# Optimization experiments

Measured on AMD Instinct MI355X. Metric: run time of the kernel, lower is better.

Reference implementation:

```python
import jax, jax.numpy as jnp
import numpy as np

BN_EPS = 1e-5


def setup_inputs() -> dict:
    key = jax.random.key(0)
    ks = jax.random.split(key, 11)
    B, C, Ci, D, H, W = 2, 256, 128, 8, 32, 32
    s = 0.02  # weight init scale
    return {
        "x": jax.random.normal(ks[0], (B, C, D, H, W), dtype=jnp.float32),
        "Wt": jax.random.normal(ks[1], (Ci, C), dtype=jnp.float32) * s,
        "bt": jax.random.normal(ks[2], (Ci,), dtype=jnp.float32) * s,
        "Wp": jax.random.normal(ks[3], (Ci, C), dtype=jnp.float32) * s,
        "bp": jax.random.normal(ks[4], (Ci,), dtype=jnp.float32) * s,
        "Wg": jax.random.normal(ks[5], (Ci, C), dtype=jnp.float32) * s,
        "bg": jax.random.normal(ks[6], (Ci,), dtype=jnp.float32) * s,
        "Ww": jax.random.normal(ks[7], (C, Ci), dtype=jnp.float32) * s,
        "bw": jax.random.normal(ks[8], (C,), dtype=jnp.float32) * s,
        "gamma": jax.random.normal(ks[9], (C,), dtype=jnp.float32),
        "beta": jax.random.normal(ks[10], (C,), dtype=jnp.float32),
    }


def reference(x, Wt, bt, Wp, bp, Wg, bg, Ww, bw, gamma, beta):
    # x: [B, C, D, H, W]; 1x1x1 Conv3d == per-position channel GEMM.
    B, C, D, H, W = x.shape
    xf = x.reshape(B, C, -1)  # [B, C, N], N = D*H*W

    theta = jnp.einsum('oc,bcn->bno', Wt, xf) + bt          # [B, N, Ci]
    phi = jnp.einsum('oc,bcn->bon', Wp, xf) + bp[None, :, None]  # [B, Ci, N]
    g = jnp.einsum('oc,bcn->bno', Wg, xf) + bg              # [B, N, Ci]

    # Unscaled, unmasked full self-attention over all N spatial positions.
    f = jnp.einsum('bnc,bcm->bnm', theta, phi)              # [B, N, N]
    a = jax.nn.softmax(f, axis=-1)
    y = jnp.einsum('bnm,bmc->bcn', a, g)                    # [B, Ci, N]

    # Output projection W: conv1x1 then BatchNorm3d (training-mode batch stats).
    wy = jnp.einsum('oc,bcn->bon', Ww, y) + bw[None, :, None]  # [B, C, N]
    mean = jnp.mean(wy, axis=(0, 2), keepdims=True)
    var = jnp.var(wy, axis=(0, 2), keepdims=True)
    wy_bn = (wy - mean) * jax.lax.rsqrt(var + BN_EPS)
    wy_bn = wy_bn * gamma[None, :, None] + beta[None, :, None]

    return wy_bn.reshape(B, C, D, H, W) + x
```

## Files before the change

kernel.cpp:

```cpp
#include <hip/hip_runtime.h>
#include <cstdint>
#include <cstddef>


typedef unsigned short u16;
typedef __bf16 bf16x8 __attribute__((ext_vector_type(8)));
typedef float f32x4 __attribute__((ext_vector_type(4)));
typedef float f32x16 __attribute__((ext_vector_type(16)));
typedef unsigned short u16x8 __attribute__((ext_vector_type(8)));

#define B_ 2
#define C_ 256
#define CI_ 128
#define N_ 8192
#define KVB 64

static __device__ __forceinline__ u16 f2bf(float f){
  unsigned u = __builtin_bit_cast(unsigned, f);
  unsigned r = (u + 0x7FFFu + ((u>>16)&1u)) >> 16;
  return (u16)r;
}
static __device__ __forceinline__ float bf2f(u16 v){
  unsigned u = ((unsigned)v) << 16;
  return __builtin_bit_cast(float, u);
}
static __device__ __forceinline__ float fexp2(float x){
  return __builtin_amdgcn_exp2f(x);
}
static __device__ __forceinline__ f32x4 f4zero(){
  f32x4 v; v[0]=0.f; v[1]=0.f; v[2]=0.f; v[3]=0.f; return v;
}
static __device__ __forceinline__ f32x16 f16zero(){
  f32x16 v;
#pragma unroll
  for (int i=0;i<16;i++) v[i]=0.f;
  return v;
}
static __device__ __forceinline__ f32x4 mfma16(bf16x8 a, bf16x8 b, f32x4 c){
  return __builtin_amdgcn_mfma_f32_16x16x32_bf16(a, b, c, 0, 0, 0);
}
static __device__ __forceinline__ f32x16 mfma32(bf16x8 a, bf16x8 b, f32x16 c){
  return __builtin_amdgcn_mfma_f32_32x32x16_bf16(a, b, c, 0, 0, 0);
}
static __device__ __forceinline__ unsigned cvtpk(float lo, float hi){
  unsigned r;
  asm("v_cvt_pk_bf16_f32 %0, %1, %2" : "=v"(r) : "v"(lo), "v"(hi));
  return r;
}
static __device__ __forceinline__ void plswap(unsigned &a, unsigned &b){
  asm volatile("v_permlane32_swap_b32 %0, %1" : "+v"(a), "+v"(b));
}

#define LOG2E 1.4426950408889634f

__global__ void k0_prep(const float* __restrict__ Wt, const float* __restrict__ Wp,
                        const float* __restrict__ Wg, const float* __restrict__ Ww,
                        const float* __restrict__ bt, const float* __restrict__ bp,
                        const float* __restrict__ bg,
                        u16* __restrict__ Wcat, u16* __restrict__ Wwb,
                        float* __restrict__ biasc, float* __restrict__ stats){
  int t = blockIdx.x*blockDim.x + threadIdx.x;
  int nthr = gridDim.x*blockDim.x;
  for (int i = t; i < 32768; i += nthr){
    Wcat[i]        = f2bf(Wt[i] * LOG2E);
    Wcat[32768+i]  = f2bf(Wp[i]);
    Wcat[65536+i]  = f2bf(Wg[i]);
    Wwb[i]         = f2bf(Ww[i]);
  }
  for (int i = t; i < 128; i += nthr){
    biasc[i] = bt[i] * LOG2E; biasc[128+i] = bp[i]; biasc[256+i] = bg[i];
  }
  for (int i = t; i < 512; i += nthr) stats[i] = 0.f;
}

__global__ __launch_bounds__(256) void k1_proj(const float* __restrict__ x,
     const u16* __restrict__ Wcat, const float* __restrict__ biasc,
     u16* __restrict__ theta, u16* __restrict__ kproj, u16* __restrict__ gT){
  __shared__ u16 At[64*264];
  __shared__ u16 Wt_[32*264];
  __shared__ u16 gbuf[32*72];
  int tid = threadIdx.x;
  int b  = blockIdx.x >> 7;
  int nb = (blockIdx.x & 127) * 64;
  int w = tid >> 6, lane = tid & 63;
  int l15 = lane & 15, kg = lane >> 4;

  {
    int cp = tid & 127, nh = tid >> 7;
    int c0 = cp*2;
    const float* src0 = x + ((size_t)(b*C_ + c0))*N_ + nb + nh*32;
    const float* src1 = src0 + N_;
#pragma unroll
    for (int j=0;j<8;j++){
      f32x4 a = *(const f32x4*)(src0 + j*4);
      f32x4 c = *(const f32x4*)(src1 + j*4);
#pragma unroll
      for (int q=0;q<4;q++){
        unsigned pk = (unsigned)f2bf(a[q]) | ((unsigned)f2bf(c[q])<<16);
        *(unsigned*)&At[(nh*32 + j*4 + q)*264 + c0] = pk;
      }
    }
  }
  __syncthreads();

  bf16x8 afr[8];
#pragma unroll
  for (int kc=0;kc<8;kc++)
    afr[kc] = *(const bf16x8*)&At[(w*16+l15)*264 + kc*32 + kg*8];

  for (int och = 0; och < 12; och++){
    {
      int o8 = tid>>3, cp8 = tid&7;
      const u16* wsrc = Wcat + ((size_t)(och*32 + o8))*256 + cp8*8;
#pragma unroll
      for (int j=0;j<4;j++)
        *(u16x8*)&Wt_[o8*264 + cp8*8 + j*64] = *(const u16x8*)(wsrc + j*64);
    }
    __syncthreads();

    f32x4 acc0 = f4zero(), acc1 = f4zero();
#pragma unroll
    for (int kc=0;kc<8;kc++){
      bf16x8 b0 = *(const bf16x8*)&Wt_[(l15)*264 + kc*32 + kg*8];
      bf16x8 b1 = *(const bf16x8*)&Wt_[(16+l15)*264 + kc*32 + kg*8];
      acc0 = mfma16(afr[kc], b0, acc0);
      acc1 = mfma16(afr[kc], b1, acc1);
    }

    if (och < 8){
      u16* dst = (och < 4) ? theta : kproj;
      int oo = (och & 3) * 32;
#pragma unroll
      for (int of=0;of<2;of++){
        int o = oo + of*16 + l15;
        float bias = biasc[och*32 + of*16 + l15];
        f32x4 acc = of ? acc1 : acc0;
#pragma unroll
        for (int i=0;i<4;i++){
          int n = nb + w*16 + kg*4 + i;
          dst[((size_t)b*N_ + n)*CI_ + o] = f2bf(acc[i] + bias);
        }
      }
      __syncthreads();
    } else {
#pragma unroll
      for (int of=0;of<2;of++){
        int o = of*16 + l15;
        float bias = biasc[och*32 + of*16 + l15];
        f32x4 acc = of ? acc1 : acc0;
#pragma unroll
        for (int i=0;i<4;i++){
          int r = w*16 + kg*4 + i;
          gbuf[o*72 + r] = f2bf(acc[i] + bias);
        }
      }
      __syncthreads();
      {
        int o = tid>>3, np = tid&7;
        int og = (och-8)*32 + o;
        u16x8 v = *(const u16x8*)&gbuf[o*72 + np*8];
        *(u16x8*)(gT + ((size_t)b*CI_ + og)*N_ + nb + np*8) = v;
      }
      __syncthreads();
    }
  }
}

__global__ __launch_bounds__(512, 2) void k2_attn(const u16* __restrict__ theta,
      const u16* __restrict__ kproj, const u16* __restrict__ gT,
      u16* __restrict__ pO, float* __restrict__ pM, float* __restrict__ pL){
  constexpr int CHUNK_N = 2048;
  constexpr int NTI = CHUNK_N / KVB;
  __shared__ char smem[65536];
  char* kbase = smem;
  char* vbase = smem + 32768;
  int tid = threadIdx.x;
  int bid = blockIdx.x;
  int combo = bid & 7;
  int b = combo & 1;
  int chunk = combo >> 1;
  int qblk = bid >> 3;
  int n0 = chunk * CHUNK_N;
  int w = tid >> 6, lane = tid & 63;
  int l31 = lane & 31, hi = lane >> 5;
  int qg = qblk*256 + w*32 + l31;

  bf16x8 qf[8];
  {
    const u16* qsrc = theta + ((size_t)b*N_ + qg)*CI_ + hi*8;
#pragma unroll
    for (int cc=0; cc<8; cc++) qf[cc] = *(const bf16x8*)(qsrc + cc*16);
  }

  int krow_s = tid >> 3, kpart = tid & 7;
  int vrow_s = tid >> 2, vpart = tid & 3;
  const u16* ksrc = kproj + ((size_t)b*N_ + n0 + krow_s)*CI_ + kpart*16;
  const u16* vsrc = gT + ((size_t)b*CI_ + vrow_s)*N_ + n0 + vpart*16;
  int kw_off[2], vw_off[2];
#pragma unroll
  for (int j=0;j<2;j++){
    int cb = kpart*32 + j*16;
    kw_off[j] = krow_s*256 + (cb ^ ((krow_s&15)<<4));
    int kb = vpart*32 + j*16;
    vw_off[j] = vrow_s*128 + (kb ^ ((vrow_s&7)<<4));
  }
  int kswz = (l31&15)<<4;
  int vswz = (l31&7)<<4;
  int kro[8], vro[4];
#pragma unroll
  for (int cc=0;cc<8;cc++) kro[cc] = l31*256 + ((cc*32 + hi*16) ^ kswz);
#pragma unroll
  for (int ks=0;ks<4;ks++) vro[ks] = l31*128 + ((ks*32 + hi*16) ^ vswz);

#pragma unroll
  for (int j=0;j<2;j++){
    *(u16x8*)(kbase + kw_off[j]) = *(const u16x8*)(ksrc + j*8);
    *(u16x8*)(vbase + vw_off[j]) = *(const u16x8*)(vsrc + j*8);
  }
  __syncthreads();

  f32x16 oacc[4];
#pragma unroll
  for (int i=0;i<4;i++) oacc[i] = f16zero();
  float mrun = -1e30f, lrun = 0.f;

  for (int t=0; t<NTI; t++){
    int cur = t & 1;
    char* kb_c = kbase + cur*16384;
    char* vb_c = vbase + cur*16384;
    u16x8 kst[2], vst[2];
    bool pf = (t+1 < NTI);
    if (pf){
      const u16* ks = ksrc + (size_t)(t+1)*KVB*CI_;
      const u16* vs = vsrc + (t+1)*KVB;
#pragma unroll
      for (int j=0;j<2;j++) kst[j] = *(const u16x8*)(ks + j*8);
#pragma unroll
      for (int j=0;j<2;j++) vst[j] = *(const u16x8*)(vs + j*8);
    }

    f32x16 sA = f16zero(), sB = f16zero();
    __builtin_amdgcn_s_setprio(1);
#pragma unroll
    for (int cc=0; cc<8; cc++){
      bf16x8 kf0 = *(const bf16x8*)(kb_c + kro[cc]);
      bf16x8 kf1 = *(const bf16x8*)(kb_c + 8192 + kro[cc]);
      sA = mfma32(kf0, qf[cc], sA);
      sB = mfma32(kf1, qf[cc], sB);
    }
    __builtin_amdgcn_s_setprio(0);

    float t8[8];
#pragma unroll
    for (int i=0;i<8;i++) t8[i] = fmaxf(fmaxf(sA[i], sA[i+8]), fmaxf(sB[i], sB[i+8]));
    float m4a = fmaxf(t8[0], t8[4]), m4b = fmaxf(t8[1], t8[5]);
    float m4c = fmaxf(t8[2], t8[6]), m4d = fmaxf(t8[3], t8[7]);
    float mx = fmaxf(fmaxf(m4a, m4b), fmaxf(m4c, m4d));
    mx = fmaxf(mx, __shfl_xor(mx, 32));
    if (__any(mx > mrun + 12.f)){
      float mnew = fmaxf(mrun, mx);
      float sc = fexp2(mrun - mnew);
      lrun *= sc;
#pragma unroll
      for (int i=0;i<4;i++)
#pragma unroll
        for (int r=0;r<16;r++) oacc[i][r] *= sc;
      mrun = mnew;
    }
    float pA[16], pB[16];
#pragma unroll
    for (int r=0;r<16;r++){ pA[r] = fexp2(sA[r]-mrun); pB[r] = fexp2(sB[r]-mrun); }
    float s8[8];
#pragma unroll
    for (int i=0;i<8;i++) s8[i] = (pA[i]+pA[i+8]) + (pB[i]+pB[i+8]);
    float s4a = s8[0]+s8[4], s4b = s8[1]+s8[5], s4c = s8[2]+s8[6], s4d = s8[3]+s8[7];
    float ps = (s4a+s4b) + (s4c+s4d);
    ps += __shfl_xor(ps, 32);
    lrun += ps;

    if (pf){
      char* kd = kbase + (cur^1)*16384;
      char* vd = vbase + (cur^1)*16384;
#pragma unroll
      for (int j=0;j<2;j++) *(u16x8*)(kd + kw_off[j]) = kst[j];
#pragma unroll
      for (int j=0;j<2;j++) *(u16x8*)(vd + vw_off[j]) = vst[j];
    }

    __builtin_amdgcn_s_setprio(1);
#pragma unroll
    for (int ks=0; ks<4; ks++){
      const float* P = (ks<2) ? pA : pB;
      int r0 = (ks&1)*8;
      unsigned a0 = cvtpk(P[r0+0], P[r0+1]);
      unsigned b0 = cvtpk(P[r0+4], P[r0+5]);
      unsigned a1 = cvtpk(P[r0+2], P[r0+3]);
      unsigned b1 = cvtpk(P[r0+6], P[r0+7]);
      plswap(a0, b0); plswap(a1, b1);
      union { unsigned u[4]; bf16x8 v; } pb;
      pb.u[0]=a0; pb.u[1]=a1; pb.u[2]=b0; pb.u[3]=b1;
#pragma unroll
      for (int c2=0; c2<4; c2++){
        bf16x8 vf = *(const bf16x8*)(vb_c + c2*4096 + vro[ks]);
        oacc[c2] = mfma32(vf, pb.v, oacc[c2]);
      }
    }
    __builtin_amdgcn_s_setprio(0);
    __syncthreads();
  }

  char* region = smem + w*8192;
#pragma unroll
  for (int c2=0;c2<4;c2++)
#pragma unroll
    for (int r=0;r<16;r++){
      int c = c2*32 + (r&3) + 8*(r>>2) + 4*hi;
      *(u16*)(region + l31*256 + ((c*2) ^ vswz)) = f2bf(oacc[c2][r]);
    }
  __syncthreads();
  {
    int ql = lane >> 1, half = lane & 1;
    int qg2 = qblk*256 + w*32 + ql;
    u16* dst = pO + ((size_t)(chunk*2 + b)*N_ + qg2)*CI_ + half*64;
    int rswz = (ql&7)<<4;
#pragma unroll
    for (int j=0;j<8;j++){
      u16x8 v2 = *(const u16x8*)(region + ql*256 + ((half*128 + j*16) ^ rswz));
      *(u16x8*)(dst + j*8) = v2;
    }
  }
  if (hi == 0){
    pM[(size_t)(chunk*2 + b)*N_ + qg] = mrun;
    pL[(size_t)(chunk*2 + b)*N_ + qg] = lrun;
  }
}

__global__ __launch_bounds__(256) void k3_wy(const u16* __restrict__ pO,
    const float* __restrict__ pM, const float* __restrict__ pL,
    const u16* __restrict__ Wwb, const float* __restrict__ bw,
    u16* __restrict__ wy, float* __restrict__ stats){
  __shared__ u16 Yt[64*136];
  __shared__ u16 Wt_[64*136];
  __shared__ float wyb[64*72];
  int tid = threadIdx.x;
  int b  = blockIdx.x >> 7;
  int nb = (blockIdx.x & 127) * 64;
  int w = tid>>6, lane = tid&63;
  int l15 = lane&15, kg = lane>>4;

  {
    int n = tid>>2, cp = tid&3;
    size_t q = (size_t)nb + n;
    float m[4], l[4];
#pragma unroll
    for (int ch=0; ch<4; ch++){
      m[ch] = pM[(size_t)(ch*2+b)*N_ + q];
      l[ch] = pL[(size_t)(ch*2+b)*N_ + q];
    }
    float M = fmaxf(fmaxf(m[0],m[1]), fmaxf(m[2],m[3]));
    float wts[4]; float L = 0.f;
#pragma unroll
    for (int ch=0; ch<4; ch++){ wts[ch] = exp2f(m[ch]-M); L += wts[ch]*l[ch]; }
    float inv = 1.f/L;
#pragma unroll
    for (int j=0;j<4;j++){
      int c0 = cp*32 + j*8;
      float acc[8];
#pragma unroll
      for (int i=0;i<8;i++) acc[i]=0.f;
#pragma unroll
      for (int ch=0; ch<4; ch++){
        u16x8 v = *(const u16x8*)(pO + ((size_t)(ch*2+b)*N_ + q)*CI_ + c0);
#pragma unroll
        for (int i=0;i<8;i++) acc[i] += wts[ch]*bf2f(v[i]);
      }
#pragma unroll
      for (int i=0;i<4;i++){
        unsigned pk = (unsigned)f2bf(acc[2*i]*inv) | ((unsigned)f2bf(acc[2*i+1]*inv)<<16);
        *(unsigned*)&Yt[n*136 + c0 + 2*i] = pk;
      }
    }
  }
  __syncthreads();

  bf16x8 afr[4];
#pragma unroll
  for (int kc=0;kc<4;kc++)
    afr[kc] = *(const bf16x8*)&Yt[(w*16+l15)*136 + kc*32 + kg*8];

  for (int oc=0; oc<4; oc++){
    {
      int o = tid>>2, cp = tid&3;
      const u16* src = Wwb + ((size_t)(oc*64 + o))*CI_ + cp*32;
#pragma unroll
      for (int j=0;j<4;j++)
        *(u16x8*)&Wt_[o*136 + cp*32 + j*8] = *(const u16x8*)(src + j*8);
    }
    __syncthreads();

    f32x4 acc[4];
#pragma unroll
    for (int of=0;of<4;of++) acc[of] = f4zero();
#pragma unroll
    for (int kc=0;kc<4;kc++){
#pragma unroll
      for (int of=0;of<4;of++){
        bf16x8 bfr = *(const bf16x8*)&Wt_[(of*16+l15)*136 + kc*32 + kg*8];
        acc[of] = mfma16(afr[kc], bfr, acc[of]);
      }
    }
#pragma unroll
    for (int of=0;of<4;of++){
#pragma unroll
      for (int i=0;i<4;i++)
        wyb[(of*16+l15)*72 + w*16 + kg*4 + i] = acc[of][i];
    }
    __syncthreads();
    {
      int o = tid>>2, np = tid&3;
      int og = oc*64 + o;
      float bias = bw[og];
      float sm = 0.f, sq = 0.f;
      u16* dst = wy + ((size_t)b*C_ + og)*N_ + nb + np*16;
      u16 buf[16];
#pragma unroll
      for (int j=0;j<4;j++){
#pragma unroll
        for (int q2=0;q2<4;q2++){
          float t2 = wyb[o*72 + np*16 + j*4 + q2] + bias;
          buf[j*4+q2] = f2bf(t2); sm += t2; sq += t2*t2;
        }
      }
      *(u16x8*)dst = *(const u16x8*)&buf[0];
      *(u16x8*)(dst+8) = *(const u16x8*)&buf[8];
      sm += __shfl_xor(sm, 1); sm += __shfl_xor(sm, 2);
      sq += __shfl_xor(sq, 1); sq += __shfl_xor(sq, 2);
      if ((tid&3)==0){
        atomicAdd(&stats[og], sm);
        atomicAdd(&stats[256+og], sq);
      }
    }
    __syncthreads();
  }
}

__global__ __launch_bounds__(256) void k4_bn(const u16* __restrict__ wy,
    const float* __restrict__ x, const float* __restrict__ stats,
    const float* __restrict__ gamma, const float* __restrict__ beta,
    float* __restrict__ out){
  size_t base = ((size_t)blockIdx.x)*2048 + (size_t)threadIdx.x*8;
  int o = (int)((base >> 13) & 255);
  const float invn = 1.f/16384.f;
  float mean = stats[o]*invn;
  float var  = stats[256+o]*invn - mean*mean;
  float rs = rsqrtf(var + 1e-5f);
  float g = gamma[o]*rs;
  float bb = beta[o];
  u16x8 a = *(const u16x8*)(wy + base);
  f32x4 x0 = *(const f32x4*)(x + base);
  f32x4 x1 = *(const f32x4*)(x + base + 4);
  f32x4 r0, r1;
#pragma unroll
  for (int q=0;q<4;q++){
    r0[q] = (bf2f(a[q])-mean)*g + bb + x0[q];
    r1[q] = (bf2f(a[4+q])-mean)*g + bb + x1[q];
  }
  *(f32x4*)(out + base)     = r0;
  *(f32x4*)(out + base + 4) = r1;
}

extern "C" void kernel_launch(void* const* d_in, const int* in_sizes, int n_in,
                              void* d_out, int out_size, void* d_ws, size_t ws_size,
                              hipStream_t stream){
  const float* x     = (const float*)d_in[0];
  const float* Wt    = (const float*)d_in[1];
  const float* bt    = (const float*)d_in[2];
  const float* Wp    = (const float*)d_in[3];
  const float* bp    = (const float*)d_in[4];
  const float* Wg    = (const float*)d_in[5];
  const float* bg    = (const float*)d_in[6];
  const float* Ww    = (const float*)d_in[7];
  const float* bw    = (const float*)d_in[8];
  const float* gamma = (const float*)d_in[9];
  const float* beta  = (const float*)d_in[10];

  char* ws = (char*)d_ws;
  u16*   theta = (u16*)(ws + 0);
  u16*   kproj = (u16*)(ws + 4194304);
  u16*   gT    = (u16*)(ws + 8388608);
  u16*   pO    = (u16*)(ws + 12582912);
  float* pM    = (float*)(ws + 29360128);
  float* pL    = (float*)(ws + 29622272);
  u16*   wy    = (u16*)(ws + 29884416);
  u16*   Wcat  = (u16*)(ws + 38273024);
  u16*   Wwb   = (u16*)(ws + 38469632);
  float* biasc = (float*)(ws + 38535168);
  float* stats = (float*)(ws + 38536704);
  float* out   = (float*)d_out;

  k0_prep<<<64, 256, 0, stream>>>(Wt, Wp, Wg, Ww, bt, bp, bg, Wcat, Wwb, biasc, stats);
  k1_proj<<<256, 256, 0, stream>>>(x, Wcat, biasc, theta, kproj, gT);
  k2_attn<<<256, 512, 0, stream>>>(theta, kproj, gT, pO, pM, pL);
  k3_wy<<<256, 256, 0, stream>>>(pO, pM, pL, Wwb, bw, wy, stats);
  k4_bn<<<2048, 256, 0, stream>>>(wy, x, stats, gamma, beta, out);
}
```

Baseline: 131.9 us.

## Software-pipeline attention loop across tiles and fold weight prep into consumers

```diff
diff --git a/kernel.cpp b/kernel.cpp
--- a/kernel.cpp
+++ b/kernel.cpp
@@ -53,29 +53,12 @@
 
 #define LOG2E 1.4426950408889634f
 
-__global__ void k0_prep(const float* __restrict__ Wt, const float* __restrict__ Wp,
-                        const float* __restrict__ Wg, const float* __restrict__ Ww,
-                        const float* __restrict__ bt, const float* __restrict__ bp,
-                        const float* __restrict__ bg,
-                        u16* __restrict__ Wcat, u16* __restrict__ Wwb,
-                        float* __restrict__ biasc, float* __restrict__ stats){
-  int t = blockIdx.x*blockDim.x + threadIdx.x;
-  int nthr = gridDim.x*blockDim.x;
-  for (int i = t; i < 32768; i += nthr){
-    Wcat[i]        = f2bf(Wt[i] * LOG2E);
-    Wcat[32768+i]  = f2bf(Wp[i]);
-    Wcat[65536+i]  = f2bf(Wg[i]);
-    Wwb[i]         = f2bf(Ww[i]);
-  }
-  for (int i = t; i < 128; i += nthr){
-    biasc[i] = bt[i] * LOG2E; biasc[128+i] = bp[i]; biasc[256+i] = bg[i];
-  }
-  for (int i = t; i < 512; i += nthr) stats[i] = 0.f;
-}
-
 __global__ __launch_bounds__(256) void k1_proj(const float* __restrict__ x,
-     const u16* __restrict__ Wcat, const float* __restrict__ biasc,
-     u16* __restrict__ theta, u16* __restrict__ kproj, u16* __restrict__ gT){
+     const float* __restrict__ Wt, const float* __restrict__ Wp,
+     const float* __restrict__ Wg, const float* __restrict__ bt,
+     const float* __restrict__ bp, const float* __restrict__ bg,
+     u16* __restrict__ theta, u16* __restrict__ kproj, u16* __restrict__ gT,
+     float* __restrict__ stats){
   __shared__ u16 At[64*264];
   __shared__ u16 Wt_[32*264];
   __shared__ u16 gbuf[32*72];
@@ -85,6 +68,10 @@
   int w = tid >> 6, lane = tid & 63;
   int l15 = lane & 15, kg = lane >> 4;
 
+  if (blockIdx.x == 0){
+    stats[tid] = 0.f; stats[256 + tid] = 0.f;
+  }
+
   {
     int cp = tid & 127, nh = tid >> 7;
     int c0 = cp*2;
@@ -111,10 +98,19 @@
   for (int och = 0; och < 12; och++){
     {
       int o8 = tid>>3, cp8 = tid&7;
-      const u16* wsrc = Wcat + ((size_t)(och*32 + o8))*256 + cp8*8;
-#pragma unroll
-      for (int j=0;j<4;j++)
-        *(u16x8*)&Wt_[o8*264 + cp8*8 + j*64] = *(const u16x8*)(wsrc + j*64);
+      const float* wsel = (och<4) ? (Wt + ((size_t)(och*32 + o8))*256)
+                        : (och<8) ? (Wp + ((size_t)((och-4)*32 + o8))*256)
+                                  : (Wg + ((size_t)((och-8)*32 + o8))*256);
+      float scl = (och<4) ? LOG2E : 1.f;
+#pragma unroll
+      for (int j=0;j<4;j++){
+        f32x4 w0 = *(const f32x4*)(wsel + cp8*8 + j*64);
+        f32x4 w1 = *(const f32x4*)(wsel + cp8*8 + j*64 + 4);
+        u16 tmp[8];
+#pragma unroll
+        for (int q=0;q<4;q++){ tmp[q] = f2bf(w0[q]*scl); tmp[4+q] = f2bf(w1[q]*scl); }
+        *(u16x8*)&Wt_[o8*264 + cp8*8 + j*64] = *(const u16x8*)tmp;
+      }
     }
     __syncthreads();
 
@@ -133,7 +129,8 @@
 #pragma unroll
       for (int of=0;of<2;of++){
         int o = oo + of*16 + l15;
-        float bias = biasc[och*32 + of*16 + l15];
+        float bias = (och<4) ? bt[och*32 + of*16 + l15] * LOG2E
+                             : bp[(och-4)*32 + of*16 + l15];
         f32x4 acc = of ? acc1 : acc0;
 #pragma unroll
         for (int i=0;i<4;i++){
@@ -146,7 +143,7 @@
 #pragma unroll
       for (int of=0;of<2;of++){
         int o = of*16 + l15;
-        float bias = biasc[och*32 + of*16 + l15];
+        float bias = bg[(och-8)*32 + of*16 + l15];
         f32x4 acc = of ? acc1 : acc0;
 #pragma unroll
         for (int i=0;i<4;i++){
@@ -171,9 +168,7 @@
       u16* __restrict__ pO, float* __restrict__ pM, float* __restrict__ pL){
   constexpr int CHUNK_N = 2048;
   constexpr int NTI = CHUNK_N / KVB;
-  __shared__ char smem[65536];
-  char* kbase = smem;
-  char* vbase = smem + 32768;
+  __shared__ char smem[81920];
   int tid = threadIdx.x;
   int bid = blockIdx.x;
   int combo = bid & 7;
@@ -185,6 +180,12 @@
   int l31 = lane & 31, hi = lane >> 5;
   int qg = qblk*256 + w*32 + l31;
 
+  char* kb_cur = smem;
+  char* kb_nxt = smem + 16384;
+  char* vb_cur = smem + 32768;
+  char* vb_nxt = smem + 49152;
+  char* vb_prev = smem + 65536;
+
   bf16x8 qf[8];
   {
     const u16* qsrc = theta + ((size_t)b*N_ + qg)*CI_ + hi*8;
@@ -214,8 +215,8 @@
 
 #pragma unroll
   for (int j=0;j<2;j++){
-    *(u16x8*)(kbase + kw_off[j]) = *(const u16x8*)(ksrc + j*8);
-    *(u16x8*)(vbase + vw_off[j]) = *(const u16x8*)(vsrc + j*8);
+    *(u16x8*)(kb_cur + kw_off[j]) = *(const u16x8*)(ksrc + j*8);
+    *(u16x8*)(vb_cur + vw_off[j]) = *(const u16x8*)(vsrc + j*8);
   }
   __syncthreads();
 
@@ -223,91 +224,108 @@
 #pragma unroll
   for (int i=0;i<4;i++) oacc[i] = f16zero();
   float mrun = -1e30f, lrun = 0.f;
-
-  for (int t=0; t<NTI; t++){
-    int cur = t & 1;
-    char* kb_c = kbase + cur*16384;
-    char* vb_c = vbase + cur*16384;
-    u16x8 kst[2], vst[2];
-    bool pf = (t+1 < NTI);
-    if (pf){
-      const u16* ks = ksrc + (size_t)(t+1)*KVB*CI_;
-      const u16* vs = vsrc + (t+1)*KVB;
-#pragma unroll
-      for (int j=0;j<2;j++) kst[j] = *(const u16x8*)(ks + j*8);
-#pragma unroll
-      for (int j=0;j<2;j++) vst[j] = *(const u16x8*)(vs + j*8);
-    }
-
-    f32x16 sA = f16zero(), sB = f16zero();
-    __builtin_amdgcn_s_setprio(1);
-#pragma unroll
-    for (int cc=0; cc<8; cc++){
-      bf16x8 kf0 = *(const bf16x8*)(kb_c + kro[cc]);
-      bf16x8 kf1 = *(const bf16x8*)(kb_c + 8192 + kro[cc]);
-      sA = mfma32(kf0, qf[cc], sA);
-      sB = mfma32(kf1, qf[cc], sB);
-    }
+  f32x16 sA0, sB0, sA1, sB1;
+
+#define K2_ROT() { char* _t = vb_prev; vb_prev = vb_cur; vb_cur = vb_nxt; vb_nxt = _t; \
+                   char* _k = kb_cur; kb_cur = kb_nxt; kb_nxt = _k; }
+
+#define K2_MAX(CA, CB) { float t8[8]; \
+    _Pragma("unroll") \
+    for (int i=0;i<8;i++) t8[i] = fmaxf(fmaxf(CA[i], CA[i+8]), fmaxf(CB[i], CB[i+8])); \
+    float mx = fmaxf(fmaxf(fmaxf(t8[0],t8[4]),fmaxf(t8[1],t8[5])), \
+                     fmaxf(fmaxf(t8[2],t8[6]),fmaxf(t8[3],t8[7]))); \
+    mx = fmaxf(mx, __shfl_xor(mx, 32)); \
+    if (__any(mx > mrun + 12.f)){ \
+      float mnew = fmaxf(mrun, mx); \
+      float sc = fexp2(mrun - mnew); \
+      lrun *= sc; \
+      _Pragma("unroll") \
+      for (int i=0;i<4;i++){ _Pragma("unroll") for (int r=0;r<16;r++) oacc[i][r] *= sc; } \
+      mrun = mnew; } }
+
+#define K2_EXP(PA, PB, pA, pB) \
+    float pA[16], pB[16]; \
+    _Pragma("unroll") \
+    for (int r=0;r<16;r++){ pA[r] = fexp2(PA[r]-mrun); pB[r] = fexp2(PB[r]-mrun); } \
+    { float s8[8]; \
+      _Pragma("unroll") \
+      for (int i=0;i<8;i++) s8[i] = (pA[i]+pA[i+8]) + (pB[i]+pB[i+8]); \
+      float ps = ((s8[0]+s8[4])+(s8[1]+s8[5])) + ((s8[2]+s8[6])+(s8[3]+s8[7])); \
+      ps += __shfl_xor(ps, 32); lrun += ps; }
+
+#define K2_PV(pA, pB) \
+    __builtin_amdgcn_s_setprio(1); \
+    _Pragma("unroll") \
+    for (int ks=0; ks<4; ks++){ \
+      const float* P = (ks<2) ? pA : pB; \
+      int r0 = (ks&1)*8; \
+      unsigned a0 = cvtpk(P[r0+0], P[r0+1]); \
+      unsigned b0 = cvtpk(P[r0+4], P[r0+5]); \
+      unsigned a1 = cvtpk(P[r0+2], P[r0+3]); \
+      unsigned b1 = cvtpk(P[r0+6], P[r0+7]); \
+      plswap(a0, b0); plswap(a1, b1); \
+      union { unsigned u[4]; bf16x8 v; } pb; \
+      pb.u[0]=a0; pb.u[1]=a1; pb.u[2]=b0; pb.u[3]=b1; \
+      _Pragma("unroll") \
+      for (int c2=0; c2<4; c2++){ \
+        bf16x8 vf = *(const bf16x8*)(vb_prev + c2*4096 + vro[ks]); \
+        oacc[c2] = mfma32(vf, pb.v, oacc[c2]); \
+      } \
+    } \
     __builtin_amdgcn_s_setprio(0);
 
-    float t8[8];
-#pragma unroll
-    for (int i=0;i<8;i++) t8[i] = fmaxf(fmaxf(sA[i], sA[i+8]), fmaxf(sB[i], sB[i+8]));
-    float m4a = fmaxf(t8[0], t8[4]), m4b = fmaxf(t8[1], t8[5]);
-    float m4c = fmaxf(t8[2], t8[6]), m4d = fmaxf(t8[3], t8[7]);
-    float mx = fmaxf(fmaxf(m4a, m4b), fmaxf(m4c, m4d));
-    mx = fmaxf(mx, __shfl_xor(mx, 32));
-    if (__any(mx > mrun + 12.f)){
-      float mnew = fmaxf(mrun, mx);
-      float sc = fexp2(mrun - mnew);
-      lrun *= sc;
-#pragma unroll
-      for (int i=0;i<4;i++)
-#pragma unroll
-        for (int r=0;r<16;r++) oacc[i][r] *= sc;
-      mrun = mnew;
-    }
-    float pA[16], pB[16];
-#pragma unroll
-    for (int r=0;r<16;r++){ pA[r] = fexp2(sA[r]-mrun); pB[r] = fexp2(sB[r]-mrun); }
-    float s8[8];
-#pragma unroll
-    for (int i=0;i<8;i++) s8[i] = (pA[i]+pA[i+8]) + (pB[i]+pB[i+8]);
-    float s4a = s8[0]+s8[4], s4b = s8[1]+s8[5], s4c = s8[2]+s8[6], s4d = s8[3]+s8[7];
-    float ps = (s4a+s4b) + (s4c+s4d);
-    ps += __shfl_xor(ps, 32);
-    lrun += ps;
-
-    if (pf){
-      char* kd = kbase + (cur^1)*16384;
-      char* vd = vbase + (cur^1)*16384;
-#pragma unroll
-      for (int j=0;j<2;j++) *(u16x8*)(kd + kw_off[j]) = kst[j];
-#pragma unroll
-      for (int j=0;j<2;j++) *(u16x8*)(vd + vw_off[j]) = vst[j];
-    }
-
-    __builtin_amdgcn_s_setprio(1);
-#pragma unroll
-    for (int ks=0; ks<4; ks++){
-      const float* P = (ks<2) ? pA : pB;
-      int r0 = (ks&1)*8;
-      unsigned a0 = cvtpk(P[r0+0], P[r0+1]);
-      unsigned b0 = cvtpk(P[r0+4], P[r0+5]);
-      unsigned a1 = cvtpk(P[r0+2], P[r0+3]);
-      unsigned b1 = cvtpk(P[r0+6], P[r0+7]);
-      plswap(a0, b0); plswap(a1, b1);
-      union { unsigned u[4]; bf16x8 v; } pb;
-      pb.u[0]=a0; pb.u[1]=a1; pb.u[2]=b0; pb.u[3]=b1;
-#pragma unroll
-      for (int c2=0; c2<4; c2++){
-        bf16x8 vf = *(const bf16x8*)(vb_c + c2*4096 + vro[ks]);
-        oacc[c2] = mfma32(vf, pb.v, oacc[c2]);
-      }
-    }
+#define K2_QKT(CA, CB) \
+    CA = f16zero(); CB = f16zero(); \
+    __builtin_amdgcn_s_setprio(1); \
+    _Pragma("unroll") \
+    for (int cc=0; cc<8; cc++){ \
+      bf16x8 kf0 = *(const bf16x8*)(kb_cur + kro[cc]); \
+      bf16x8 kf1 = *(const bf16x8*)(kb_cur + 8192 + kro[cc]); \
+      CA = mfma32(kf0, qf[cc], CA); \
+      CB = mfma32(kf1, qf[cc], CB); \
+    } \
     __builtin_amdgcn_s_setprio(0);
+
+#define K2_LOADS(T) \
+    int tn = ((T)+1 < NTI) ? ((T)+1) : (NTI-1); \
+    u16x8 kst0 = *(const u16x8*)(ksrc + (size_t)tn*KVB*CI_); \
+    u16x8 kst1 = *(const u16x8*)(ksrc + (size_t)tn*KVB*CI_ + 8); \
+    u16x8 vst0 = *(const u16x8*)(vsrc + tn*KVB); \
+    u16x8 vst1 = *(const u16x8*)(vsrc + tn*KVB + 8);
+
+#define K2_WRITES() \
+    *(u16x8*)(kb_nxt + kw_off[0]) = kst0; *(u16x8*)(kb_nxt + kw_off[1]) = kst1; \
+    *(u16x8*)(vb_nxt + vw_off[0]) = vst0; *(u16x8*)(vb_nxt + vw_off[1]) = vst1;
+
+#define K2_ITER(T, CA, CB, PA, PB) { \
+    K2_LOADS(T) \
+    K2_QKT(CA, CB) \
+    K2_EXP(PA, PB, pA_, pB_) \
+    K2_WRITES() \
+    K2_PV(pA_, pB_) \
+    K2_MAX(CA, CB) \
+    __syncthreads(); \
+    K2_ROT() }
+
+  {
+    K2_LOADS(0)
+    K2_QKT(sA0, sB0)
+    K2_WRITES()
+    K2_MAX(sA0, sB0)
     __syncthreads();
-  }
+    K2_ROT()
+  }
+  for (int t = 1; t < NTI-1; t += 2){
+    K2_ITER(t,   sA1, sB1, sA0, sB0)
+    K2_ITER(t+1, sA0, sB0, sA1, sB1)
+  }
+  K2_ITER(NTI-1, sA1, sB1, sA0, sB0)
+
+  {
+    K2_EXP(sA1, sB1, pA_, pB_)
+    K2_PV(pA_, pB_)
+  }
+  __syncthreads();
 
   char* region = smem + w*8192;
 #pragma unroll
@@ -337,7 +355,7 @@
 
 __global__ __launch_bounds__(256) void k3_wy(const u16* __restrict__ pO,
     const float* __restrict__ pM, const float* __restrict__ pL,
-    const u16* __restrict__ Wwb, const float* __restrict__ bw,
+    const float* __restrict__ Ww, const float* __restrict__ bw,
     u16* __restrict__ wy, float* __restrict__ stats){
   __shared__ u16 Yt[64*136];
   __shared__ u16 Wt_[64*136];
@@ -391,10 +409,16 @@
   for (int oc=0; oc<4; oc++){
     {
       int o = tid>>2, cp = tid&3;
-      const u16* src = Wwb + ((size_t)(oc*64 + o))*CI_ + cp*32;
-#pragma unroll
-      for (int j=0;j<4;j++)
-        *(u16x8*)&Wt_[o*136 + cp*32 + j*8] = *(const u16x8*)(src + j*8);
+      const float* src = Ww + ((size_t)(oc*64 + o))*CI_ + cp*32;
+#pragma unroll
+      for (int j=0;j<4;j++){
+        f32x4 w0 = *(const f32x4*)(src + j*8);
+        f32x4 w1 = *(const f32x4*)(src + j*8 + 4);
+        u16 tmp[8];
+#pragma unroll
+        for (int q2=0;q2<4;q2++){ tmp[q2] = f2bf(w0[q2]); tmp[4+q2] = f2bf(w1[q2]); }
+        *(u16x8*)&Wt_[o*136 + cp*32 + j*8] = *(const u16x8*)tmp;
+      }
     }
     __syncthreads();
 
@@ -492,15 +516,11 @@
   float* pM    = (float*)(ws + 29360128);
   float* pL    = (float*)(ws + 29622272);
   u16*   wy    = (u16*)(ws + 29884416);
-  u16*   Wcat  = (u16*)(ws + 38273024);
-  u16*   Wwb   = (u16*)(ws + 38469632);
-  float* biasc = (float*)(ws + 38535168);
-  float* stats = (float*)(ws + 38536704);
+  float* stats = (float*)(ws + 38273024);
   float* out   = (float*)d_out;
 
-  k0_prep<<<64, 256, 0, stream>>>(Wt, Wp, Wg, Ww, bt, bp, bg, Wcat, Wwb, biasc, stats);
-  k1_proj<<<256, 256, 0, stream>>>(x, Wcat, biasc, theta, kproj, gT);
+  k1_proj<<<256, 256, 0, stream>>>(x, Wt, Wp, Wg, bt, bp, bg, theta, kproj, gT, stats);
   k2_attn<<<256, 512, 0, stream>>>(theta, kproj, gT, pO, pM, pL);
-  k3_wy<<<256, 256, 0, stream>>>(pO, pM, pL, Wwb, bw, wy, stats);
+  k3_wy<<<256, 256, 0, stream>>>(pO, pM, pL, Ww, bw, wy, stats);
   k4_bn<<<2048, 256, 0, stream>>>(wy, x, stats, gamma, beta, out);
 }
```

Result: no change. 131.1 us (-0.6%).
